# Optimization experiments

Hardware: AMD Instinct MI355X
Metric: run time of the kernel (lower is better)

The kernel has to match this reference:

```python
import jax, jax.numpy as jnp
import numpy as np

N_HEAD = 16
EPS = 1e-6


def setup_inputs() -> dict:
    key = jax.random.key(0)
    ks = jax.random.split(key, 5)
    B, T, C = 2, 2048, 1024
    hd = C // N_HEAD
    x = jax.random.normal(ks[0], (B, T, C), dtype=jnp.float32)
    # rotary frequencies (unit-magnitude complex, decomposed into cos/sin)
    theta = 10000.0 ** (-np.arange(0, hd, 2, dtype=np.float32) / hd)  # [hd/2]
    ang = np.arange(T, dtype=np.float32)[:, None] * theta[None, :]    # [T, hd/2]
    freqs_cos = jnp.asarray(np.cos(ang))
    freqs_sin = jnp.asarray(np.sin(ang))
    w_attn = jax.random.normal(ks[1], (3 * C, C), dtype=jnp.float32) * 0.02
    w_proj = jax.random.normal(ks[2], (C, C), dtype=jnp.float32) * 0.02
    q_norm_w = jnp.ones((hd,), dtype=jnp.float32)
    k_norm_w = jnp.ones((hd,), dtype=jnp.float32)
    return {"x": x, "freqs_cos": freqs_cos, "freqs_sin": freqs_sin,
            "w_attn": w_attn, "w_proj": w_proj,
            "q_norm_w": q_norm_w, "k_norm_w": k_norm_w}


def _rmsnorm(x, w):
    # x: [..., hd]; per-last-dim RMSNorm with learned scale
    rms = jax.lax.rsqrt(jnp.mean(x * x, axis=-1, keepdims=True) + EPS)
    return x * rms * w


def _rope(x, cos, sin):
    # x: [B, T, H, hd]; cos/sin: [T, hd/2] -> broadcast [1, T, 1, hd/2]
    x2 = x.reshape(*x.shape[:-1], -1, 2)  # [B,T,H,hd/2,2]
    x0, x1 = x2[..., 0], x2[..., 1]
    c = cos[None, :, None, :]
    s = sin[None, :, None, :]
    r0 = x0 * c - x1 * s
    r1 = x0 * s + x1 * c
    return jnp.stack([r0, r1], axis=-1).reshape(x.shape)


def reference(x, freqs_cos, freqs_sin, w_attn, w_proj, q_norm_w, k_norm_w):
    B, T, C = x.shape
    H = N_HEAD
    hd = C // H
    qkv = x @ w_attn.T  # [B, T, 3C]
    q, k, v = jnp.split(qkv, 3, axis=-1)
    q = q.reshape(B, T, H, hd)
    k = k.reshape(B, T, H, hd)
    v = v.reshape(B, T, H, hd)
    q = _rmsnorm(q, q_norm_w)
    k = _rmsnorm(k, k_norm_w)
    q = _rope(q, freqs_cos[:T], freqs_sin[:T])
    k = _rope(k, freqs_cos[:T], freqs_sin[:T])
    scale = 1.0 / jnp.sqrt(jnp.asarray(hd, dtype=x.dtype))
    # causal SDPA: scores [B, H, T, T]
    scores = jnp.einsum('bihd,bjhd->bhij', q, k) * scale
    causal = jnp.tril(jnp.ones((T, T), dtype=bool))
    scores = jnp.where(causal[None, None], scores, jnp.finfo(scores.dtype).min)
    p = jax.nn.softmax(scores, axis=-1)
    y = jnp.einsum('bhij,bjhd->bihd', p, v).reshape(B, T, C)
    return y @ w_proj.T
```

## Files before the change

### kernel.cpp

```cpp
#include <hip/hip_runtime.h>

typedef unsigned short u16;
typedef unsigned int u32;
typedef __bf16 bf16x8 __attribute__((ext_vector_type(8)));
typedef float f32x4 __attribute__((ext_vector_type(4)));

__device__ __forceinline__ u16 f2bf(float f) {
    union { float f; u32 u; } v;
    v.f = f;
    u32 r = v.u + 0x7fffu + ((v.u >> 16) & 1u);
    return (u16)(r >> 16);
}

__device__ __forceinline__ u32 fbits(float f) {
    union { float f; u32 u; } v; v.f = f; return v.u;
}

__device__ __forceinline__ void glds16(const void* g, void* l) {
    __builtin_amdgcn_global_load_lds(
        (__attribute__((address_space(1))) unsigned int*)(g),
        (__attribute__((address_space(3))) unsigned int*)(l), 16, 0, 0);
}

#define MFMA __builtin_amdgcn_mfma_f32_16x16x32_bf16

__global__ void castbf3(const float* __restrict__ a, u16* __restrict__ oa,
                        const float* __restrict__ b, u16* __restrict__ ob,
                        const float* __restrict__ c, u16* __restrict__ oc,
                        const float* __restrict__ fcos, const float* __restrict__ fsin,
                        float2* __restrict__ csb) {
    int blk = blockIdx.x;
    if (blk < 4096) {
        int i = blk * 256 + threadIdx.x;
        float4 v = ((const float4*)a)[i];
        ushort4 o;
        o.x = f2bf(v.x); o.y = f2bf(v.y); o.z = f2bf(v.z); o.w = f2bf(v.w);
        ((ushort4*)oa)[i] = o;
    } else if (blk < 7168) {
        int i = (blk - 4096) * 256 + threadIdx.x;
        int n = i >> 8, c4 = i & 255;
        int np;
        if (n < 2048) {
            int part = n >> 10, rem = n & 1023;
            int h = rem >> 6, d = rem & 63;
            int nd = (d >> 1) + ((d & 1) << 5);
            np = part * 1024 + h * 64 + nd;
        } else np = n;
        float4 v = ((const float4*)b)[i];
        ushort4 o;
        o.x = f2bf(v.x); o.y = f2bf(v.y); o.z = f2bf(v.z); o.w = f2bf(v.w);
        ((ushort4*)ob)[np * 256 + c4] = o;
    } else if (blk < 8192) {
        int i = (blk - 7168) * 256 + threadIdx.x;
        float4 v = ((const float4*)c)[i];
        ushort4 o;
        o.x = f2bf(v.x); o.y = f2bf(v.y); o.z = f2bf(v.z); o.w = f2bf(v.w);
        ((ushort4*)oc)[i] = o;
    } else {
        int i = (blk - 8192) * 256 + threadIdx.x;
        csb[i] = make_float2(fcos[i], fsin[i]);
    }
}

__global__ __launch_bounds__(256) void gemm_qkv(
    const u16* __restrict__ A, const u16* __restrict__ B,
    const float2* __restrict__ csb,
    const float* __restrict__ qw, const float* __restrict__ kw,
    u16* __restrict__ q, u16* __restrict__ k, u16* __restrict__ vt)
{
    __shared__ alignas(16) u16 SB[2 * 8192];
    u16* Es = SB;
    const int tid = threadIdx.x;
    const int lane = tid & 63;
    const int wave = tid >> 6;
    const int bm = blockIdx.y * 128, bn = blockIdx.x * 128;
    const int wm = (wave >> 1) * 64, wn = (wave & 1) * 64;
    const int ln = lane & 15, quad = lane >> 4;
    const int K = 1024;

    f32x4 acc[4][4] = {};

    const int srow = tid >> 2;
    const int scol = (tid & 3) * 8;
    const u16* gA = A + (size_t)(bm + srow) * K + scol;
    const u16* gB = B + (size_t)(bn + srow) * K + scol;

    auto stage = [&](int k0, int bf) {
        u16* lA = &SB[bf * 8192 + wave * 512];
        u16* lB = &SB[bf * 8192 + 4096 + wave * 512];
        glds16(gA + k0, lA);
        glds16(gA + (size_t)64 * K + k0, lA + 2048);
        glds16(gB + k0, lB);
        glds16(gB + (size_t)64 * K + k0, lB + 2048);
    };

    stage(0, 0);
    for (int it = 0; it < 32; ++it) {
        stage((((it + 1) & 31) << 5), (it + 1) & 1);
        asm volatile("s_waitcnt vmcnt(4)\n\ts_barrier" ::: "memory");

        const u16* Asb = &SB[(it & 1) * 8192];
        const u16* Bsb = Asb + 4096;
        bf16x8 af[4], bfr[4];
#pragma unroll
        for (int i = 0; i < 4; ++i)
            af[i] = *(const bf16x8*)&Asb[(wm + i * 16 + ln) * 32 + quad * 8];
#pragma unroll
        for (int j = 0; j < 4; ++j)
            bfr[j] = *(const bf16x8*)&Bsb[(wn + j * 16 + ln) * 32 + quad * 8];
#pragma unroll
        for (int i = 0; i < 4; ++i)
#pragma unroll
            for (int j = 0; j < 4; ++j)
                acc[i][j] = MFMA(af[i], bfr[j], acc[i][j], 0, 0, 0);

        asm volatile("s_barrier" ::: "memory");
    }
    asm volatile("s_waitcnt vmcnt(0)\n\ts_barrier" ::: "memory");

    const int part = bn >> 10;
    const int headw = wave & 1;
    const int h0 = (bn & 1023) >> 6;
    const float SC = 0.18033688011112042f;
    const int b = bm >> 11, tbase = bm & 2047;

    if (part == 2) {
#pragma unroll
        for (int i = 0; i < 4; ++i) {
            int tlb = wm + i * 16 + quad * 4;
#pragma unroll
            for (int j = 0; j < 4; ++j) {
                int d = j * 16 + ln;
                uint2 pk;
                pk.x = __builtin_amdgcn_perm(fbits(acc[i][j][1]), fbits(acc[i][j][0]), 0x07060302u);
                pk.y = __builtin_amdgcn_perm(fbits(acc[i][j][3]), fbits(acc[i][j][2]), 0x07060302u);
                *(uint2*)&Es[headw * 8192 + d * 128 + (tlb ^ (ln << 3))] = pk;
            }
        }
        __syncthreads();
#pragma unroll
        for (int c = 0; c < 8; ++c) {
            int cid = c * 256 + tid;
            int tc = cid & 15, d = (cid >> 4) & 63, hd = cid >> 10;
            uint4 v = *(const uint4*)&Es[hd * 8192 + d * 128 + ((tc ^ (d & 15)) << 3)];
            size_t dst = ((size_t)((b * 16 + h0 + hd) * 64 + d)) * 2048
                       + tbase + ((tc >> 3) << 6) + (((tc & 7) ^ (d & 7)) << 3);
            *(uint4*)&vt[dst] = v;
        }
        return;
    }

    const float* nw = (part == 0) ? qw : kw;
    float wv[4];
#pragma unroll
    for (int j = 0; j < 4; ++j) {
        int nd = j * 16 + ln;
        int od = ((nd & 31) << 1) | (nd >> 5);
        wv[j] = nw[od];
    }

    if (part == 0) {
#pragma unroll
        for (int i = 0; i < 4; ++i) {
            float oj[4][4];
#pragma unroll
            for (int r = 0; r < 4; ++r) {
                int tloc = wm + i * 16 + quad * 4 + r;
                int t = (bm + tloc) & 2047;
                float v0 = acc[i][0][r], v1 = acc[i][1][r];
                float v2 = acc[i][2][r], v3 = acc[i][3][r];
                float ss = v0 * v0 + v1 * v1 + v2 * v2 + v3 * v3;
                ss += __shfl_xor(ss, 1);
                ss += __shfl_xor(ss, 2);
                ss += __shfl_xor(ss, 4);
                ss += __shfl_xor(ss, 8);
                float g = rsqrtf(ss * (1.0f / 64.0f) + 1e-6f) * SC;
                float x0a = v0 * g * wv[0], x0b = v1 * g * wv[1];
                float x1a = v2 * g * wv[2], x1b = v3 * g * wv[3];
                float2 cs0 = csb[t * 32 + ln];
                float2 cs1 = csb[t * 32 + 16 + ln];
                oj[0][r] = x0a * cs0.x - x1a * cs0.y;
                oj[2][r] = x0a * cs0.y + x1a * cs0.x;
                oj[1][r] = x0b * cs1.x - x1b * cs1.y;
                oj[3][r] = x0b * cs1.y + x1b * cs1.x;
            }
            int tlb = wm + i * 16 + quad * 4;
#pragma unroll
            for (int j = 0; j < 4; ++j) {
                uint2 pk;
                pk.x = __builtin_amdgcn_perm(fbits(oj[j][1]), fbits(oj[j][0]), 0x07060302u);
                pk.y = __builtin_amdgcn_perm(fbits(oj[j][3]), fbits(oj[j][2]), 0x07060302u);
                *(uint2*)&Es[headw * 8192 + (j * 16 + ln) * 128 + (tlb ^ (ln << 3))] = pk;
            }
        }
        __syncthreads();
#pragma unroll
        for (int c = 0; c < 8; ++c) {
            int cid = c * 256 + tid;
            int tc = cid & 15, d = (cid >> 4) & 63, hd = cid >> 10;
            uint4 v = *(const uint4*)&Es[hd * 8192 + d * 128 + ((tc ^ (d & 15)) << 3)];
            size_t dst = ((size_t)((b * 16 + h0 + hd) * 64 + d)) * 2048 + tbase + tc * 8;
            *(uint4*)&q[dst] = v;
        }
        return;
    }

#pragma unroll
    for (int i = 0; i < 4; ++i) {
#pragma unroll
        for (int r = 0; r < 4; ++r) {
            int tloc = wm + i * 16 + quad * 4 + r;
            int t = (bm + tloc) & 2047;

            float v0 = acc[i][0][r], v1 = acc[i][1][r];
            float v2 = acc[i][2][r], v3 = acc[i][3][r];
            float ss = v0 * v0 + v1 * v1 + v2 * v2 + v3 * v3;
            ss += __shfl_xor(ss, 1);
            ss += __shfl_xor(ss, 2);
            ss += __shfl_xor(ss, 4);
            ss += __shfl_xor(ss, 8);
            float g = rsqrtf(ss * (1.0f / 64.0f) + 1e-6f);

            float x0a = v0 * g * wv[0], x0b = v1 * g * wv[1];
            float x1a = v2 * g * wv[2], x1b = v3 * g * wv[3];
            float2 cs0 = csb[t * 32 + ln];
            float2 cs1 = csb[t * 32 + 16 + ln];
            float o0 = x0a * cs0.x - x1a * cs0.y;
            float o2 = x0a * cs0.y + x1a * cs0.x;
            float o1 = x0b * cs1.x - x1b * cs1.y;
            float o3 = x0b * cs1.y + x1b * cs1.x;

            u16* e = &Es[headw * 8192 + tloc * 64 + ln];
            e[((0 ^ quad) << 4)] = f2bf(o0);
            e[((1 ^ quad) << 4)] = f2bf(o1);
            e[((2 ^ quad) << 4)] = f2bf(o2);
            e[((3 ^ quad) << 4)] = f2bf(o3);
        }
    }
    __syncthreads();
#pragma unroll
    for (int c = 0; c < 8; ++c) {
        int cid = c * 256 + tid;
        int dc = cid & 7, tloc = (cid >> 3) & 127, hd = cid >> 10;
        int q2 = (tloc >> 2) & 3;
        int sq = (dc >> 1) ^ q2;
        uint4 v = *(const uint4*)&Es[hd * 8192 + tloc * 64 + sq * 16 + (dc & 1) * 8];
        int gm = bm + tloc;
        int bb = gm >> 11, t = gm & 2047;
        size_t rb = ((size_t)((bb * 16 + h0 + hd) * 2048 + t)) * 64;
        *(uint4*)&k[rb + ((dc ^ (t & 7)) << 3)] = v;
    }
}

__global__ __launch_bounds__(256) void gemm64(
    const u16* __restrict__ A, const u16* __restrict__ B,
    float* __restrict__ C, int M, int N, int K)
{
    __shared__ alignas(16) u16 SB[2 * 6144];
    const int tid = threadIdx.x;
    const int lane = tid & 63;
    const int wave = tid >> 6;
    const int bm = blockIdx.y * 64, bn = blockIdx.x * 128;
    const int wm = (wave >> 1) * 32, wn = (wave & 1) * 64;
    const int ln = lane & 15, quad = lane >> 4;

    f32x4 acc[2][4] = {};

    const int srow = tid >> 2;
    const int scol = (tid & 3) * 8;
    const u16* gA = A + (size_t)(bm + srow) * K + scol;
    const u16* gB = B + (size_t)(bn + srow) * K + scol;

    auto stage = [&](int k0, int bf) {
        u16* lA = &SB[bf * 6144 + wave * 512];
        u16* lB = &SB[bf * 6144 + 2048 + wave * 512];
        glds16(gA + k0, lA);
        glds16(gB + k0, lB);
        glds16(gB + (size_t)64 * K + k0, lB + 2048);
    };

    stage(0, 0);
    for (int it = 0; it < 32; ++it) {
        stage((((it + 1) & 31) << 5), (it + 1) & 1);
        asm volatile("s_waitcnt vmcnt(3)\n\ts_barrier" ::: "memory");

        const u16* Asb = &SB[(it & 1) * 6144];
        const u16* Bsb = Asb + 2048;
        bf16x8 af[2], bfr[4];
#pragma unroll
        for (int i = 0; i < 2; ++i)
            af[i] = *(const bf16x8*)&Asb[(wm + i * 16 + ln) * 32 + quad * 8];
#pragma unroll
        for (int j = 0; j < 4; ++j)
            bfr[j] = *(const bf16x8*)&Bsb[(wn + j * 16 + ln) * 32 + quad * 8];
#pragma unroll
        for (int i = 0; i < 2; ++i)
#pragma unroll
            for (int j = 0; j < 4; ++j)
                acc[i][j] = MFMA(af[i], bfr[j], acc[i][j], 0, 0, 0);

        asm volatile("s_barrier" ::: "memory");
    }

#pragma unroll
    for (int i = 0; i < 2; ++i) {
#pragma unroll
        for (int r = 0; r < 4; ++r) {
            int gm = bm + wm + i * 16 + quad * 4 + r;
            float* Crow = C + (size_t)gm * N + bn + wn + ln;
#pragma unroll
            for (int j = 0; j < 4; ++j)
                Crow[j * 16] = acc[i][j][r];
        }
    }
}

__global__ __launch_bounds__(512) void attn_kernel(
    const u16* __restrict__ Q, const u16* __restrict__ K,
    const u16* __restrict__ VT, u16* __restrict__ Y)
{
    __shared__ alignas(16) u16 Ks[2][64 * 64];
    __shared__ alignas(16) u16 Vs[2][64 * 64];
    __shared__ alignas(16) u16 Ps[8][16 * 80];

    const int tid = threadIdx.x;
    const int lane = tid & 63;
    const int wave = tid >> 6;
    const int ln = lane & 15, quad = lane >> 4;
    const int pi = blockIdx.x;
    const int bh = blockIdx.y;
    const int qaIdx = pi, qbIdx = 31 - pi;
    const bool isB = wave >= 4;
    const int qidx = isB ? qbIdx : qaIdx;
    const int myq = qidx * 64 + (wave & 3) * 16;
    const size_t base = (size_t)bh * 2048 * 64;
    const u16* Kg = K + base;
    const u16* Vg = VT + base;
    const __bf16* Qg = (const __bf16*)(Q + base);

    const int qt = myq + ln;
    bf16x8 qf0, qf1;
#pragma unroll
    for (int j = 0; j < 8; ++j) {
        qf0[j] = Qg[(size_t)(quad * 8 + j) * 2048 + qt];
        qf1[j] = Qg[(size_t)(32 + quad * 8 + j) * 2048 + qt];
    }

    f32x4 o[4] = {};
    float l = 0.0f;
    const int nstages = qbIdx + 1;
    const int sw = ln & 7;
    const int srow = wave * 8 + (lane >> 3);
    const int scol = (lane & 7) * 8;
    u16* Psw = &Ps[wave][0];

    auto prefetch = [&](int jb, int nb) {
        glds16(&Kg[(size_t)(jb + srow) * 64 + scol], &Ks[nb][wave * 512]);
        glds16(&Vg[(size_t)srow * 2048 + jb + scol], &Vs[nb][wave * 512]);
    };
    prefetch(0, 0);

    for (int jt = 0; jt < nstages; ++jt) {
        const int jbn = (jt + 1 < nstages) ? (jt + 1) * 64 : 0;
        prefetch(jbn, (jt + 1) & 1);
        asm volatile("s_waitcnt vmcnt(2)\n\ts_barrier" ::: "memory");

        const u16* ksb = &Ks[jt & 1][0];
        const u16* vsb = &Vs[jt & 1][0];

        if (isB || jt <= qaIdx) {
            f32x4 st[4];
#pragma unroll
            for (int ct = 0; ct < 4; ++ct) {
                bf16x8 kf0 = *(const bf16x8*)&ksb[(ct * 16 + ln) * 64 + ((0 + quad) ^ sw) * 8];
                bf16x8 kf1 = *(const bf16x8*)&ksb[(ct * 16 + ln) * 64 + ((4 + quad) ^ sw) * 8];
                f32x4 z = {};
                z = MFMA(kf0, qf0, z, 0, 0, 0);
                st[ct] = MFMA(kf1, qf1, z, 0, 0, 0);
            }
            if (jt == qidx) {
                const int qg = myq + ln;
                const int jb = jt * 64;
#pragma unroll
                for (int ct = 0; ct < 4; ++ct)
#pragma unroll
                    for (int r = 0; r < 4; ++r)
                        if (jb + ct * 16 + quad * 4 + r > qg) st[ct][r] = -1e30f;
            }

            float sum = 0.0f;
#pragma unroll
            for (int ct = 0; ct < 4; ++ct) {
                float e0 = exp2f(st[ct][0]), e1 = exp2f(st[ct][1]);
                float e2 = exp2f(st[ct][2]), e3 = exp2f(st[ct][3]);
                sum += (e0 + e1) + (e2 + e3);
                uint2 pk;
                pk.x = __builtin_amdgcn_perm(fbits(e1), fbits(e0), 0x07060302u);
                pk.y = __builtin_amdgcn_perm(fbits(e3), fbits(e2), 0x07060302u);
                *(uint2*)&Psw[ln * 80 + ct * 16 + quad * 4] = pk;
            }
            sum += __shfl_xor(sum, 16);
            sum += __shfl_xor(sum, 32);
            l += sum;

            __builtin_amdgcn_s_waitcnt(0xC07F);
            bf16x8 pf0 = *(const bf16x8*)&Psw[ln * 80 + quad * 8];
            bf16x8 pf1 = *(const bf16x8*)&Psw[ln * 80 + 32 + quad * 8];

#pragma unroll
            for (int dt = 0; dt < 4; ++dt) {
                bf16x8 vf0 = *(const bf16x8*)&vsb[(dt * 16 + ln) * 64 + ((0 + quad) ^ sw) * 8];
                bf16x8 vf1 = *(const bf16x8*)&vsb[(dt * 16 + ln) * 64 + ((4 + quad) ^ sw) * 8];
                o[dt] = MFMA(pf0, vf0, o[dt], 0, 0, 0);
                o[dt] = MFMA(pf1, vf1, o[dt], 0, 0, 0);
            }
        }
        asm volatile("s_waitcnt lgkmcnt(0)\n\ts_barrier" ::: "memory");
    }

    const int b = bh >> 4, h = bh & 15;
#pragma unroll
    for (int r = 0; r < 4; ++r) {
        float lr = __shfl(l, (lane & 48) + quad * 4 + r);
        float inv = 1.0f / lr;
        int gq = myq + quad * 4 + r;
        size_t yb = ((size_t)(b * 2048 + gq)) * 1024 + h * 64 + ln;
#pragma unroll
        for (int dt = 0; dt < 4; ++dt)
            Y[yb + dt * 16] = f2bf(o[dt][r] * inv);
    }
}

extern "C" void kernel_launch(void* const* d_in, const int* in_sizes, int n_in,
                              void* d_out, int out_size, void* d_ws, size_t ws_size,
                              hipStream_t stream) {
    const float* x      = (const float*)d_in[0];
    const float* fcos   = (const float*)d_in[1];
    const float* fsin   = (const float*)d_in[2];
    const float* w_attn = (const float*)d_in[3];
    const float* w_proj = (const float*)d_in[4];
    const float* qw     = (const float*)d_in[5];
    const float* kw     = (const float*)d_in[6];
    float* out = (float*)d_out;

    char* ws = (char*)d_ws;
    u16*    xb  = (u16*)(ws + 0);
    u16*    yb  = (u16*)(ws + 0);
    u16*    wab = (u16*)(ws + 8388608);
    u16*    wpb = (u16*)(ws + 14680064);
    u16*    qb  = (u16*)(ws + 16777216);
    u16*    kb  = (u16*)(ws + 25165824);
    u16*    vtb = (u16*)(ws + 33554432);
    float2* csb = (float2*)(ws + 41943040);

    castbf3<<<8448, 256, 0, stream>>>(x, xb, w_attn, wab, w_proj, wpb, fcos, fsin, csb);

    gemm_qkv<<<dim3(24, 32), 256, 0, stream>>>(xb, wab, csb, qw, kw, qb, kb, vtb);

    attn_kernel<<<dim3(16, 32), 512, 0, stream>>>(qb, kb, vtb, yb);

    gemm64<<<dim3(8, 64), 256, 0, stream>>>(yb, wpb, out, 4096, 1024, 1024);
}
```

Measured before the change: 193.0 us.

## Software-pipeline QK^T of next tile with PV of current tile in attention

Restructures the attention inner loop so the S=QK^T MFMAs for the next K tile are issued after the barrier and overlap with the exp/P write and PV MFMAs of the current tile. It also defers the cross-lane row-sum shuffles of l until after the loop instead of doing them every iteration. This trades extra live registers for the pipelined score tile, and a full vmcnt(0) wait per iteration, for better overlap of MFMA work with the softmax exponentials.

Result: faster. 187.8 us (-2.7%).

```diff
diff --git a/kernel.cpp b/kernel.cpp
--- a/kernel.cpp
+++ b/kernel.cpp
@@ -358,36 +358,37 @@
         glds16(&Kg[(size_t)(jb + srow) * 64 + scol], &Ks[nb][wave * 512]);
         glds16(&Vg[(size_t)srow * 2048 + jb + scol], &Vs[nb][wave * 512]);
     };
+    auto computeS = [&](f32x4* st, const u16* ksb) {
+#pragma unroll
+        for (int ct = 0; ct < 4; ++ct) {
+            bf16x8 kf0 = *(const bf16x8*)&ksb[(ct * 16 + ln) * 64 + (quad ^ sw) * 8];
+            bf16x8 kf1 = *(const bf16x8*)&ksb[(ct * 16 + ln) * 64 + ((4 + quad) ^ sw) * 8];
+            f32x4 z = {};
+            z = MFMA(kf0, qf0, z, 0, 0, 0);
+            st[ct] = MFMA(kf1, qf1, z, 0, 0, 0);
+        }
+    };
+    auto applyMask = [&](f32x4* st, int jb) {
+        const int qg = myq + ln;
+#pragma unroll
+        for (int ct = 0; ct < 4; ++ct)
+#pragma unroll
+            for (int r = 0; r < 4; ++r)
+                if (jb + ct * 16 + quad * 4 + r > qg) st[ct][r] = -1e30f;
+    };
+
     prefetch(0, 0);
+    asm volatile("s_waitcnt vmcnt(0)\n\ts_barrier" ::: "memory");
+    f32x4 st[4];
+    computeS(st, &Ks[0][0]);
+    if (qidx == 0) applyMask(st, 0);
 
     for (int jt = 0; jt < nstages; ++jt) {
-        const int jbn = (jt + 1 < nstages) ? (jt + 1) * 64 : 0;
-        prefetch(jbn, (jt + 1) & 1);
-        asm volatile("s_waitcnt vmcnt(2)\n\ts_barrier" ::: "memory");
-
-        const u16* ksb = &Ks[jt & 1][0];
-        const u16* vsb = &Vs[jt & 1][0];
-
-        if (isB || jt <= qaIdx) {
-            f32x4 st[4];
-#pragma unroll
-            for (int ct = 0; ct < 4; ++ct) {
-                bf16x8 kf0 = *(const bf16x8*)&ksb[(ct * 16 + ln) * 64 + ((0 + quad) ^ sw) * 8];
-                bf16x8 kf1 = *(const bf16x8*)&ksb[(ct * 16 + ln) * 64 + ((4 + quad) ^ sw) * 8];
-                f32x4 z = {};
-                z = MFMA(kf0, qf0, z, 0, 0, 0);
-                st[ct] = MFMA(kf1, qf1, z, 0, 0, 0);
-            }
-            if (jt == qidx) {
-                const int qg = myq + ln;
-                const int jb = jt * 64;
-#pragma unroll
-                for (int ct = 0; ct < 4; ++ct)
-#pragma unroll
-                    for (int r = 0; r < 4; ++r)
-                        if (jb + ct * 16 + quad * 4 + r > qg) st[ct][r] = -1e30f;
-            }
-
+        const bool haveNext = (jt + 1 < nstages);
+        if (haveNext) prefetch((jt + 1) * 64, (jt + 1) & 1);
+
+        const bool curActive = isB || jt <= qaIdx;
+        if (curActive) {
             float sum = 0.0f;
 #pragma unroll
             for (int ct = 0; ct < 4; ++ct) {
@@ -399,17 +400,25 @@
                 pk.y = __builtin_amdgcn_perm(fbits(e3), fbits(e2), 0x07060302u);
                 *(uint2*)&Psw[ln * 80 + ct * 16 + quad * 4] = pk;
             }
-            sum += __shfl_xor(sum, 16);
-            sum += __shfl_xor(sum, 32);
             l += sum;
-
+        }
+
+        asm volatile("s_waitcnt vmcnt(0)\n\ts_barrier" ::: "memory");
+
+        const bool nextActive = haveNext && (isB || (jt + 1) <= qaIdx);
+        if (nextActive) {
+            computeS(st, &Ks[(jt + 1) & 1][0]);
+            if (jt + 1 == qidx) applyMask(st, (jt + 1) * 64);
+        }
+
+        if (curActive) {
             __builtin_amdgcn_s_waitcnt(0xC07F);
             bf16x8 pf0 = *(const bf16x8*)&Psw[ln * 80 + quad * 8];
             bf16x8 pf1 = *(const bf16x8*)&Psw[ln * 80 + 32 + quad * 8];
-
+            const u16* vsb = &Vs[jt & 1][0];
 #pragma unroll
             for (int dt = 0; dt < 4; ++dt) {
-                bf16x8 vf0 = *(const bf16x8*)&vsb[(dt * 16 + ln) * 64 + ((0 + quad) ^ sw) * 8];
+                bf16x8 vf0 = *(const bf16x8*)&vsb[(dt * 16 + ln) * 64 + (quad ^ sw) * 8];
                 bf16x8 vf1 = *(const bf16x8*)&vsb[(dt * 16 + ln) * 64 + ((4 + quad) ^ sw) * 8];
                 o[dt] = MFMA(pf0, vf0, o[dt], 0, 0, 0);
                 o[dt] = MFMA(pf1, vf1, o[dt], 0, 0, 0);
@@ -417,6 +426,9 @@
         }
         asm volatile("s_waitcnt lgkmcnt(0)\n\ts_barrier" ::: "memory");
     }
+
+    l += __shfl_xor(l, 16);
+    l += __shfl_xor(l, 32);
 
     const int b = bh >> 4, h = bh & 15;
 #pragma unroll
```
